# Kernel optimization log

Measured on AMD Instinct MI355X. Metric: run time of the kernel, lower is better.

Reference implementation:

```python
import jax, jax.numpy as jnp
import numpy as np

EPS = 1e-5
GRID = 128          # coarse grid extent -> fine grid is 256^3
N1 = 15000          # coarse voxels
CHILD = 4           # children kept per coarse voxel
N2 = N1 * CHILD     # fine voxels
CIN = 128
COUT = 64


def _build_geometry():
    rng = np.random.RandomState(0)
    flat = rng.choice(GRID ** 3, N1, replace=False)
    cc = np.stack(np.unravel_index(flat, (GRID, GRID, GRID)), axis=1)  # [N1,3]
    offs8 = np.array([[i, j, k] for i in (0, 1) for j in (0, 1) for k in (0, 1)], dtype=np.int64)
    kidx = np.argsort(rng.rand(N1, 8), axis=1)[:, :CHILD]              # [N1,4] distinct child taps
    fine = (cc[:, None, :] * 2 + offs8[kidx]).reshape(-1, 3)           # [N2,3] unique fine coords
    up_src = np.repeat(np.arange(N1), CHILD).astype(np.int32)
    up_kidx = kidx.reshape(-1).astype(np.int32)
    # 27-offset neighbor maps via hashed coordinate lookup
    key = (fine[:, 0] * 256 + fine[:, 1]) * 256 + fine[:, 2]
    order = np.argsort(key)
    skey = key[order]
    offs27 = np.array([[i, j, k] for i in (-1, 0, 1) for j in (-1, 0, 1) for k in (-1, 0, 1)], dtype=np.int64)
    nbr_src = np.full((27, N2), N2, dtype=np.int32)
    nbr_dst = np.full((27, N2), N2, dtype=np.int32)
    for t in range(27):
        q = fine + offs27[t]
        inb = np.all((q >= 0) & (q < 256), axis=1)
        qk = (q[:, 0] * 256 + q[:, 1]) * 256 + q[:, 2]
        pos = np.searchsorted(skey, qk)
        pos = np.clip(pos, 0, N2 - 1)
        hit = inb & (skey[pos] == qk)
        nbr_src[t, hit] = order[pos[hit]]
        nbr_dst[t, hit] = np.arange(N2, dtype=np.int32)[hit]
    return up_src, up_kidx, nbr_src, nbr_dst


def setup_inputs() -> dict:
    key = jax.random.key(0)
    ks = jax.random.split(key, 8)
    up_src, up_kidx, nbr_src, nbr_dst = _build_geometry()
    s_up = 1.0 / np.sqrt(CIN * 8)
    s1 = 1.0 / np.sqrt(CIN * 27)
    s2 = 1.0 / np.sqrt(COUT * 27)
    return {
        "feats1": jax.random.normal(ks[0], (N1, CIN), jnp.float32),
        "feats2": jax.random.normal(ks[1], (N2, CIN // 2), jnp.float32),
        "w_up": jax.random.normal(ks[2], (8, CIN, CIN // 2), jnp.float32) * s_up,
        "gamma_up": jnp.ones((CIN // 2,), jnp.float32),
        "beta_up": jnp.zeros((CIN // 2,), jnp.float32),
        "w1": jax.random.normal(ks[3], (27, CIN, COUT), jnp.float32) * s1,
        "gamma1": jnp.ones((COUT,), jnp.float32),
        "beta1": jnp.zeros((COUT,), jnp.float32),
        "w2": jax.random.normal(ks[4], (27, COUT, COUT), jnp.float32) * s2,
        "gamma2": jnp.ones((COUT,), jnp.float32),
        "beta2": jnp.zeros((COUT,), jnp.float32),
        "up_src": jnp.asarray(up_src),
        "up_kidx": jnp.asarray(up_kidx),
        "nbr_src": jnp.asarray(nbr_src),
        "nbr_dst": jnp.asarray(nbr_dst),
    }


def _bn_relu(x, gamma, beta):
    # training-mode BatchNorm over the point dimension (biased variance), then ReLU
    m = jnp.mean(x, axis=0)
    v = jnp.var(x, axis=0)
    return jax.nn.relu((x - m) * jax.lax.rsqrt(v + EPS) * gamma + beta)


def _sparse_conv(x, w, nbr_src, nbr_dst):
    # x: [N,Ci]; w: [27,Ci,Co]; transform-then-gather-scatter (hash-map sparse conv)
    n = x.shape[0]
    co = w.shape[-1]
    y = jnp.einsum("nc,kco->kno", x, w)                       # [27,N,Co]
    y = jnp.concatenate([y, jnp.zeros((27, 1, co), y.dtype)], axis=1)  # sentinel row
    msg = jnp.take_along_axis(y, nbr_src[:, :, None], axis=1)  # [27,N,Co]
    out = jnp.zeros((n + 1, co), y.dtype).at[nbr_dst.reshape(-1)].add(msg.reshape(-1, co))
    return out[:-1]


def reference(feats1, feats2, w_up, gamma_up, beta_up, w1, gamma1, beta1, w2,
              gamma2, beta2, up_src, up_kidx, nbr_src, nbr_dst):
    # transposed conv k=2 s=2, generative=False: each fine voxel pulls from its unique coarse parent
    y = jnp.einsum("mc,kco->kmo", feats1, w_up)               # [8,N1,Cin/2]
    x1 = y[up_kidx, up_src]                                   # [N2,Cin/2]
    x1 = _bn_relu(x1, gamma_up, beta_up)
    x = jnp.concatenate([x1, feats2], axis=-1)                # [N2,Cin]
    h = _bn_relu(_sparse_conv(x, w1, nbr_src, nbr_dst), gamma1, beta1)
    return _bn_relu(_sparse_conv(h, w2, nbr_src, nbr_dst), gamma2, beta2)
```

## Files before the change

kernel.cpp:

```cpp
#include <hip/hip_runtime.h>


typedef short bf16x4 __attribute__((ext_vector_type(4)));
typedef short bf16x8 __attribute__((ext_vector_type(8)));
typedef float f32x16 __attribute__((ext_vector_type(16)));

__device__ __forceinline__ short f2bf(float f) {
    unsigned u = __float_as_uint(f);
    u += 0x7fffu + ((u >> 16) & 1u);
    return (short)(u >> 16);
}
__device__ __forceinline__ float bf2f(short s) {
    return __uint_as_float(((unsigned)(unsigned short)s) << 16);
}

__global__ __launch_bounds__(256) void k_setup(
    const float* __restrict__ w_up, const float* __restrict__ f1,
    const int* __restrict__ up_kidx,
    short* __restrict__ wupp, short* __restrict__ f1bf,
    int* __restrict__ pmask, int* __restrict__ perm_rows,
    int* __restrict__ rank, int* __restrict__ cnt,
    int n1, int nbGeom)
{
    int tid = threadIdx.x;
    int bid = blockIdx.x;
    if (bid < nbGeom) {
        int p = bid * 256 + tid;
        if (p >= n1) return;
        int4 kd = *(const int4*)(up_kidx + 4 * p);
        int a = kd.x * 4 + 0, b = kd.y * 4 + 1, c = kd.z * 4 + 2, d = kd.w * 4 + 3;
        int t;
        if (a > b) { t = a; a = b; b = t; }
        if (c > d) { t = c; c = d; d = t; }
        if (a > c) { t = a; a = c; c = t; }
        if (b > d) { t = b; b = d; d = t; }
        if (b > c) { t = b; b = c; c = t; }
        perm_rows[4 * p + 0] = 4 * p + (a & 3);
        perm_rows[4 * p + 1] = 4 * p + (b & 3);
        perm_rows[4 * p + 2] = 4 * p + (c & 3);
        perm_rows[4 * p + 3] = 4 * p + (d & 3);
        int mask = (1 << (a >> 2)) | (1 << (b >> 2)) | (1 << (c >> 2)) | (1 << (d >> 2));
        pmask[p] = mask;
        rank[p] = atomicAdd(&cnt[mask], 1);
    } else {
        const int nup8 = 8192;
        int tot = nup8 + n1 * 16;
        int gs = (gridDim.x - nbGeom) * 256;
        for (int e8 = (bid - nbGeom) * 256 + tid; e8 < tot; e8 += gs) {
            if (e8 < nup8) {
                int l = e8 & 63, nt = (e8 >> 6) & 15, ks = e8 >> 10;
                int kb = ks * 16 + (l >> 5) * 8;
                int col = nt * 32 + (l & 31);
                const float* src = w_up + (size_t)(col >> 6) * 8192 + (size_t)kb * 64 + (col & 63);
                bf16x8 o;
                #pragma unroll
                for (int j = 0; j < 8; ++j) o[j] = f2bf(src[(size_t)j * 64]);
                *(bf16x8*)(wupp + (size_t)e8 * 8) = o;
            } else {
                int g = e8 - nup8;
                const float* src = f1 + (size_t)g * 8;
                float4 a = *(const float4*)src;
                float4 b = *(const float4*)(src + 4);
                bf16x8 o;
                o[0] = f2bf(a.x); o[1] = f2bf(a.y); o[2] = f2bf(a.z); o[3] = f2bf(a.w);
                o[4] = f2bf(b.x); o[5] = f2bf(b.y); o[6] = f2bf(b.z); o[7] = f2bf(b.w);
                *(bf16x8*)(f1bf + (size_t)g * 8) = o;
            }
        }
    }
}

__global__ __launch_bounds__(256) void k_up(
    const short* __restrict__ f1bf, const short* __restrict__ wupp,
    const int* __restrict__ pmask, const int* __restrict__ cnt,
    const int* __restrict__ rank, int* __restrict__ perm_par,
    int4* __restrict__ tiles, int* __restrict__ ntl,
    short* __restrict__ yup8, float* __restrict__ stats,
    const float* __restrict__ w1, const float* __restrict__ w2,
    short* __restrict__ w1p, short* __restrict__ w2p,
    const int* __restrict__ nbr, int2* __restrict__ ext,
    int* __restrict__ extc, float* __restrict__ y1, float* __restrict__ y2,
    int n1, int n2, int nt, int nbExt)
{
    int gemmEnd = 1 + 2 * nt;
    if (blockIdx.x == 0) {
        __shared__ int sA[256], sB[256], bb[256];
        int t = threadIdx.x;
        int c = cnt[t], tc = (c + 31) >> 5;
        sA[t] = c; sB[t] = tc;
        __syncthreads();
        for (int off = 1; off < 256; off <<= 1) {
            int a = (t >= off) ? sA[t - off] : 0;
            int b = (t >= off) ? sB[t - off] : 0;
            __syncthreads();
            sA[t] += a; sB[t] += b;
            __syncthreads();
        }
        int base = sA[t] - c, toff = sB[t] - tc;
        bb[t] = base;
        for (int j = 0; j < tc; ++j) tiles[toff + j] = make_int4(t, base, j * 32, c);
        if (t == 255) ntl[0] = sB[255];
        __syncthreads();
        for (int p = t; p < n1; p += 256)
            perm_par[bb[pmask[p]] + rank[p]] = p;
        return;
    }
    if (blockIdx.x >= gemmEnd) {
        int ab = blockIdx.x - gemmEnd;
        int tid = threadIdx.x;
        if (ab < 256) {
            long long tot = (long long)n2 * 16;
            float4 z = make_float4(0.f, 0.f, 0.f, 0.f);
            for (long long e = (long long)ab * 256 + tid; e < tot; e += 256LL * 256) {
                ((float4*)y1)[e] = z;
                ((float4*)y2)[e] = z;
            }
        } else if (ab < 320) {
            const int nw18 = 27648, tot = 27648 + 13824;
            for (int e8 = (ab - 256) * 256 + tid; e8 < tot; e8 += 64 * 256) {
                if (e8 < nw18) {
                    int l = e8 & 63, ch = (e8 >> 6) & 1, ks = (e8 >> 7) & 7, t = e8 >> 10;
                    int kb = ks * 16 + (l >> 5) * 8;
                    int col = ch * 32 + (l & 31);
                    const float* src = w1 + (size_t)t * 8192 + (size_t)kb * 64 + col;
                    bf16x8 o;
                    #pragma unroll
                    for (int j = 0; j < 8; ++j) o[j] = f2bf(src[(size_t)j * 64]);
                    *(bf16x8*)(w1p + (size_t)e8 * 8) = o;
                } else {
                    int g = e8 - nw18;
                    int l = g & 63, ch = (g >> 6) & 1, ks = (g >> 7) & 3, t = g >> 9;
                    int kb = ks * 16 + (l >> 5) * 8;
                    int col = ch * 32 + (l & 31);
                    const float* src = w2 + (size_t)t * 4096 + (size_t)kb * 64 + col;
                    bf16x8 o;
                    #pragma unroll
                    for (int j = 0; j < 8; ++j) o[j] = f2bf(src[(size_t)j * 64]);
                    *(bf16x8*)(w2p + (size_t)g * 8) = o;
                }
            }
        } else {
            int i = (ab - 320) * 256 + tid;
            unsigned hm = 0;
            if (i < n2) {
                #pragma unroll
                for (int t = 0; t < 27; ++t) {
                    int s = nbr[(size_t)t * n2 + i];
                    if (s < n2 && (s >> 2) != (i >> 2)) hm |= 1u << t;
                }
            }
            __shared__ int lcnt, lbase;
            if (tid == 0) lcnt = 0;
            __syncthreads();
            int nh = __popc(hm);
            int myofs = 0;
            if (nh) myofs = atomicAdd(&lcnt, nh);
            __syncthreads();
            if (tid == 0 && lcnt) lbase = atomicAdd(extc, lcnt);
            __syncthreads();
            if (nh) {
                int pos = lbase + myofs;
                unsigned m = hm;
                while (m) {
                    int t = __ffs(m) - 1;
                    m &= m - 1;
                    int s = nbr[(size_t)t * n2 + i];
                    ext[pos++] = make_int2(i, s | (t << 16));
                }
            }
        }
        return;
    }
    __shared__ short lds[32 * 136];
    __shared__ float bs[64], bq[64];
    int bid = blockIdx.x - 1;
    int tile = bid >> 1;
    int w = threadIdx.x >> 6, lane = threadIdx.x & 63;
    int na = (bid & 1) * 8 + w, nb = na + 4;
    if (threadIdx.x < 64) { bs[threadIdx.x] = 0.f; bq[threadIdx.x] = 0.f; }
    #pragma unroll
    for (int it = 0; it < 2; ++it) {
        int c = it * 256 + threadIdx.x;
        int row = c >> 4, col8 = c & 15;
        int gr = tile * 32 + row; if (gr >= n1) gr = n1 - 1;
        int4 g = *(const int4*)(f1bf + (size_t)gr * 128 + col8 * 8);
        short* d = &lds[row * 136 + col8 * 8];
        *(int2*)d = make_int2(g.x, g.y);
        *(int2*)(d + 4) = make_int2(g.z, g.w);
    }
    int m = lane & 31, half = lane >> 5;
    int pm_l = (tile * 32 + m < n1) ? pmask[tile * 32 + m] : 0;
    __syncthreads();
    f32x16 a0, a1;
    #pragma unroll
    for (int i = 0; i < 16; ++i) { a0[i] = 0.f; a1[i] = 0.f; }
    const bf16x8* bp = (const bf16x8*)wupp;
    #pragma unroll
    for (int ks = 0; ks < 8; ++ks) {
        const short* ap = &lds[m * 136 + ks * 16 + half * 8];
        bf16x4 lo = *(const bf16x4*)ap, hi = *(const bf16x4*)(ap + 4);
        bf16x8 a = __builtin_shufflevector(lo, hi, 0, 1, 2, 3, 4, 5, 6, 7);
        bf16x8 b0 = bp[(size_t)(ks * 16 + na) * 64 + lane];
        bf16x8 b1 = bp[(size_t)(ks * 16 + nb) * 64 + lane];
        a0 = __builtin_amdgcn_mfma_f32_32x32x16_bf16(a, b0, a0, 0, 0, 0);
        a1 = __builtin_amdgcn_mfma_f32_32x32x16_bf16(a, b1, a1, 0, 0, 0);
    }
    int col = lane & 31;
    #pragma unroll
    for (int pass = 0; pass < 2; ++pass) {
        const f32x16& acc = pass ? a1 : a0;
        int n = pass ? nb : na;
        int slot = n >> 1, c = (n & 1) * 32 + col;
        float s0 = 0.f, q0 = 0.f;
        #pragma unroll
        for (int reg = 0; reg < 16; ++reg) {
            int r = (reg & 3) + 8 * (reg >> 2) + 4 * half;
            int p = tile * 32 + r;
            float v = acc[reg];
            int mk = __shfl(pm_l, r);
            if (p < n1) {
                yup8[(size_t)p * 512 + n * 32 + col] = f2bf(v);
                if ((mk >> slot) & 1) { s0 += v; q0 += v * v; }
            }
        }
        s0 += __shfl_xor(s0, 32);
        q0 += __shfl_xor(q0, 32);
        if (lane < 32) { atomicAdd(&bs[c], s0); atomicAdd(&bq[c], q0); }
    }
    __syncthreads();
    if (threadIdx.x < 64) {
        atomicAdd(&stats[threadIdx.x], bs[threadIdx.x]);
        atomicAdd(&stats[64 + threadIdx.x], bq[threadIdx.x]);
    }
}

__global__ __launch_bounds__(256) void k_extA(
    const short* __restrict__ yup8, const float* __restrict__ f2,
    const int* __restrict__ up_kidx, const float* __restrict__ w1,
    const float* __restrict__ gamma, const float* __restrict__ beta,
    const float* __restrict__ stats, const int2* __restrict__ ext,
    const int* __restrict__ extc, float* __restrict__ y, int n2)
{
    __shared__ float sc[64], sh[64];
    int tid = threadIdx.x;
    if (tid < 64) {
        float inv = 1.0f / (float)n2;
        float mean = stats[tid] * inv;
        float var = stats[64 + tid] * inv - mean * mean;
        float s = gamma[tid] * rsqrtf(var + 1e-5f);
        sc[tid] = s; sh[tid] = beta[tid] - mean * s;
    }
    __syncthreads();
    int gw = (blockIdx.x * 256 + tid) >> 6;
    int nw = (gridDim.x * 256) >> 6;
    int c = tid & 63;
    int ec = extc[0];
    for (int e = gw; e < ec; e += nw) {
        int2 en = ext[e];
        int i = en.x, s = en.y & 0xFFFF, t = en.y >> 16;
        const short* xr = yup8 + (size_t)(s >> 2) * 512 + up_kidx[s] * 64;
        const float* fr = f2 + (size_t)s * 64;
        const float* wr = w1 + (size_t)t * 8192 + c;
        float acc = 0.f;
        #pragma unroll 4
        for (int k = 0; k < 64; ++k) {
            float xk = fmaxf(bf2f(xr[k]) * sc[k] + sh[k], 0.f);
            acc += xk * wr[(size_t)k * 64];
        }
        #pragma unroll 4
        for (int k = 0; k < 64; ++k)
            acc += fr[k] * wr[(size_t)(64 + k) * 64];
        atomicAdd(&y[(size_t)i * 64 + c], acc);
    }
}

__global__ __launch_bounds__(256) void k_extB(
    const float* __restrict__ y1, const float* __restrict__ w2,
    const float* __restrict__ gamma, const float* __restrict__ beta,
    const float* __restrict__ stats, const int2* __restrict__ ext,
    const int* __restrict__ extc, float* __restrict__ y, int n2)
{
    __shared__ float sc[64], sh[64];
    int tid = threadIdx.x;
    if (tid < 64) {
        float inv = 1.0f / (float)n2;
        float mean = stats[tid] * inv;
        float var = stats[64 + tid] * inv - mean * mean;
        float s = gamma[tid] * rsqrtf(var + 1e-5f);
        sc[tid] = s; sh[tid] = beta[tid] - mean * s;
    }
    __syncthreads();
    int gw = (blockIdx.x * 256 + tid) >> 6;
    int nw = (gridDim.x * 256) >> 6;
    int c = tid & 63;
    int ec = extc[0];
    for (int e = gw; e < ec; e += nw) {
        int2 en = ext[e];
        int i = en.x, s = en.y & 0xFFFF, t = en.y >> 16;
        const float* hr = y1 + (size_t)s * 64;
        const float* wr = w2 + (size_t)t * 4096 + c;
        float acc = 0.f;
        #pragma unroll 4
        for (int k = 0; k < 64; ++k) {
            float hk = fmaxf(hr[k] * sc[k] + sh[k], 0.f);
            acc += hk * wr[(size_t)k * 64];
        }
        atomicAdd(&y[(size_t)i * 64 + c], acc);
    }
}

__device__ __forceinline__ void pair_epi2(const f32x16& a0v, const f32x16& a1v,
                                          int outrow0, int outrow1, int lane,
                                          int ch, float* __restrict__ y,
                                          float* __restrict__ bs,
                                          float* __restrict__ bq)
{
    int col = lane & 31;
    int c = ch * 32 + col;
    int r0[16], r1[16];
    #pragma unroll
    for (int reg = 0; reg < 16; ++reg) {
        int r = (reg & 3) + 8 * (reg >> 2) + 4 * (lane >> 5);
        r0[reg] = __shfl(outrow0, r);
        r1[reg] = __shfl(outrow1, r);
    }
    float o0[16], o1[16];
    #pragma unroll
    for (int reg = 0; reg < 16; ++reg) {
        int ra = (r0[reg] >= 0) ? r0[reg] : 0;
        int rb = (r1[reg] >= 0) ? r1[reg] : 0;
        o0[reg] = y[(size_t)ra * 64 + c];
        o1[reg] = y[(size_t)rb * 64 + c];
    }
    float s0 = 0.f, q0 = 0.f;
    #pragma unroll
    for (int reg = 0; reg < 16; ++reg) {
        if (r0[reg] >= 0) {
            float v = a0v[reg] + o0[reg];
            y[(size_t)r0[reg] * 64 + c] = v;
            s0 += v; q0 += v * v;
        }
        if (r1[reg] >= 0) {
            float v = a1v[reg] + o1[reg];
            y[(size_t)r1[reg] * 64 + c] = v;
            s0 += v; q0 += v * v;
        }
    }
    s0 += __shfl_xor(s0, 32);
    q0 += __shfl_xor(q0, 32);
    if (lane < 32) { atomicAdd(&bs[c], s0); atomicAdd(&bq[c], q0); }
}

__device__ __forceinline__ int tap27(int pa, int pb) {
    int di = ((pb >> 2) & 1) - ((pa >> 2) & 1);
    int dj = ((pb >> 1) & 1) - ((pa >> 1) & 1);
    int dk = (pb & 1) - (pa & 1);
    return (di + 1) * 9 + (dj + 1) * 3 + (dk + 1);
}

__global__ __launch_bounds__(256) void k_pairA(
    const short* __restrict__ yup8, const float* __restrict__ f2,
    const int* __restrict__ up_kidx, const short* __restrict__ wp,
    const float* __restrict__ gamma, const float* __restrict__ beta,
    const float* __restrict__ stats, const int* __restrict__ perm_par,
    const int* __restrict__ perm_rows, const int4* __restrict__ tiles,
    const int* __restrict__ n_tiles, float* __restrict__ y,
    float* __restrict__ ostats, int n2)
{
    constexpr int LP = 520;
    __shared__ short lds[32 * LP];
    __shared__ int srows[128], soff[128];
    __shared__ float scs[64], shs[64], bs[64], bq[64];
    int bt = blockIdx.x;
    if (bt >= n_tiles[0]) return;
    int4 td = tiles[bt];
    int mask = td.x, p_start = td.y, lt = td.z, cntb = td.w;
    int tid = threadIdx.x;
    if (tid < 128) {
        int li = lt + (tid >> 2);
        int pid = perm_par[p_start + ((li < cntb) ? li : 0)];
        int i = perm_rows[pid * 4 + (tid & 3)];
        srows[tid] = i;
        soff[tid] = (i >> 2) * 512 + up_kidx[i] * 64;
    } else if (tid < 192) {
        int cc = tid - 128;
        float inv = 1.0f / (float)n2;
        float mean = stats[cc] * inv;
        float var = stats[64 + cc] * inv - mean * mean;
        float s = gamma[cc] * rsqrtf(var + 1e-5f);
        scs[cc] = s; shs[cc] = beta[cc] - mean * s;
    } else {
        int cc = tid - 192;
        bs[cc] = 0.f; bq[cc] = 0.f;
    }
    __syncthreads();
    #pragma unroll
    for (int it = 0; it < 8; ++it) {
        int c0 = it * 256 + tid;
        int pl = c0 >> 6, w8 = c0 & 63;
        int j = w8 >> 4, col8 = w8 & 15;
        short* d = &lds[pl * LP + j * 128 + col8 * 8];
        if (col8 < 8) {
            bf16x8 g = *(const bf16x8*)(yup8 + (size_t)soff[pl * 4 + j] + col8 * 8);
            short o[8];
            #pragma unroll
            for (int u = 0; u < 8; ++u) {
                int cc = col8 * 8 + u;
                o[u] = f2bf(fmaxf(bf2f(g[u]) * scs[cc] + shs[cc], 0.f));
            }
            *(int2*)d = make_int2(((int)(unsigned short)o[0]) | ((int)o[1] << 16),
                                  ((int)(unsigned short)o[2]) | ((int)o[3] << 16));
            *(int2*)(d + 4) = make_int2(((int)(unsigned short)o[4]) | ((int)o[5] << 16),
                                        ((int)(unsigned short)o[6]) | ((int)o[7] << 16));
        } else {
            const float* fr = f2 + (size_t)srows[pl * 4 + j] * 64 + (col8 - 8) * 8;
            float4 f0 = *(const float4*)fr;
            float4 f1v = *(const float4*)(fr + 4);
            short o[8] = {f2bf(f0.x), f2bf(f0.y), f2bf(f0.z), f2bf(f0.w),
                          f2bf(f1v.x), f2bf(f1v.y), f2bf(f1v.z), f2bf(f1v.w)};
            *(int2*)d = make_int2(((int)(unsigned short)o[0]) | ((int)o[1] << 16),
                                  ((int)(unsigned short)o[2]) | ((int)o[3] << 16));
            *(int2*)(d + 4) = make_int2(((int)(unsigned short)o[4]) | ((int)o[5] << 16),
                                        ((int)(unsigned short)o[6]) | ((int)o[7] << 16));
        }
    }
    int p0 = -1, p1 = -1, p2 = -1, p3 = -1;
    #pragma unroll
    for (int b = 7; b >= 0; --b)
        if ((mask >> b) & 1) { p3 = p2; p2 = p1; p1 = p0; p0 = b; }
    int w = tid >> 6, lane = tid & 63;
    int a0 = w >> 1, a1 = a0 + 2, ch = w & 1;
    int pa0 = (a0 == 0) ? p0 : p1;
    int pa1 = (a1 == 2) ? p2 : p3;
    int t00 = tap27(pa0, p0), t01 = tap27(pa0, p1), t02 = tap27(pa0, p2), t03 = tap27(pa0, p3);
    int t10 = tap27(pa1, p0), t11 = tap27(pa1, p1), t12 = tap27(pa1, p2), t13 = tap27(pa1, p3);
    int m = lane & 31, half = lane >> 5;
    int li = lt + m;
    bool vp = li < cntb;
    int pid = perm_par[p_start + (vp ? li : 0)];
    int outrow0 = vp ? perm_rows[pid * 4 + a0] : -1;
    int outrow1 = vp ? perm_rows[pid * 4 + a1] : -1;
    __syncthreads();
    f32x16 acc0, acc1;
    #pragma unroll
    for (int i = 0; i < 16; ++i) { acc0[i] = 0.f; acc1[i] = 0.f; }
    const bf16x8* bp = (const bf16x8*)wp;
    #pragma unroll
    for (int b = 0; b < 4; ++b) {
        int tb0 = (b == 0) ? t00 : (b == 1) ? t01 : (b == 2) ? t02 : t03;
        int tb1 = (b == 0) ? t10 : (b == 1) ? t11 : (b == 2) ? t12 : t13;
        #pragma unroll
        for (int kk = 0; kk < 8; ++kk) {
            int ks = b * 8 + kk;
            const short* ap = &lds[m * LP + ks * 16 + half * 8];
            bf16x4 lo = *(const bf16x4*)ap, hi = *(const bf16x4*)(ap + 4);
            bf16x8 a = __builtin_shufflevector(lo, hi, 0, 1, 2, 3, 4, 5, 6, 7);
            bf16x8 b0 = bp[((size_t)(tb0 * 8 + kk) * 2 + ch) * 64 + lane];
            bf16x8 b1 = bp[((size_t)(tb1 * 8 + kk) * 2 + ch) * 64 + lane];
            acc0 = __builtin_amdgcn_mfma_f32_32x32x16_bf16(a, b0, acc0, 0, 0, 0);
            acc1 = __builtin_amdgcn_mfma_f32_32x32x16_bf16(a, b1, acc1, 0, 0, 0);
        }
    }
    pair_epi2(acc0, acc1, outrow0, outrow1, lane, ch, y, bs, bq);
    __syncthreads();
    if (tid < 64) {
        atomicAdd(&ostats[tid], bs[tid]);
        atomicAdd(&ostats[64 + tid], bq[tid]);
    }
}

__global__ __launch_bounds__(256) void k_pairB(
    const float* __restrict__ y1, const short* __restrict__ wp,
    const float* __restrict__ gamma, const float* __restrict__ beta,
    const float* __restrict__ stats, const int* __restrict__ perm_par,
    const int* __restrict__ perm_rows, const int4* __restrict__ tiles,
    const int* __restrict__ n_tiles, float* __restrict__ y,
    float* __restrict__ ostats, int n2)
{
    constexpr int LP = 264;
    __shared__ short lds[32 * LP];
    __shared__ int srows[128];
    __shared__ float scs[64], shs[64], bs[64], bq[64];
    int bt = blockIdx.x;
    if (bt >= n_tiles[0]) return;
    int4 td = tiles[bt];
    int mask = td.x, p_start = td.y, lt = td.z, cntb = td.w;
    int tid = threadIdx.x;
    if (tid < 128) {
        int li = lt + (tid >> 2);
        int pid = perm_par[p_start + ((li < cntb) ? li : 0)];
        srows[tid] = perm_rows[pid * 4 + (tid & 3)];
    } else if (tid < 192) {
        int cc = tid - 128;
        float inv = 1.0f / (float)n2;
        float mean = stats[cc] * inv;
        float var = stats[64 + cc] * inv - mean * mean;
        float s = gamma[cc] * rsqrtf(var + 1e-5f);
        scs[cc] = s; shs[cc] = beta[cc] - mean * s;
    } else {
        int cc = tid - 192;
        bs[cc] = 0.f; bq[cc] = 0.f;
    }
    __syncthreads();
    #pragma unroll
    for (int it = 0; it < 4; ++it) {
        int c0 = it * 256 + tid;
        int pl = c0 >> 5, w8 = c0 & 31;
        int j = w8 >> 3, col8 = w8 & 7;
        const float* fr = y1 + (size_t)srows[pl * 4 + j] * 64 + col8 * 8;
        float4 f0 = *(const float4*)fr;
        float4 f1v = *(const float4*)(fr + 4);
        short o[8];
        #pragma unroll
        for (int u = 0; u < 4; ++u) {
            int cc = col8 * 8 + u;
            float v = (u == 0) ? f0.x : (u == 1) ? f0.y : (u == 2) ? f0.z : f0.w;
            o[u] = f2bf(fmaxf(v * scs[cc] + shs[cc], 0.f));
        }
        #pragma unroll
        for (int u = 0; u < 4; ++u) {
            int cc = col8 * 8 + 4 + u;
            float v = (u == 0) ? f1v.x : (u == 1) ? f1v.y : (u == 2) ? f1v.z : f1v.w;
            o[4 + u] = f2bf(fmaxf(v * scs[cc] + shs[cc], 0.f));
        }
        short* d = &lds[pl * LP + j * 64 + col8 * 8];
        *(int2*)d = make_int2(((int)(unsigned short)o[0]) | ((int)o[1] << 16),
                              ((int)(unsigned short)o[2]) | ((int)o[3] << 16));
        *(int2*)(d + 4) = make_int2(((int)(unsigned short)o[4]) | ((int)o[5] << 16),
                                    ((int)(unsigned short)o[6]) | ((int)o[7] << 16));
    }
    int p0 = -1, p1 = -1, p2 = -1, p3 = -1;
    #pragma unroll
    for (int b = 7; b >= 0; --b)
        if ((mask >> b) & 1) { p3 = p2; p2 = p1; p1 = p0; p0 = b; }
    int w = tid >> 6, lane = tid & 63;
    int a0 = w >> 1, a1 = a0 + 2, ch = w & 1;
    int pa0 = (a0 == 0) ? p0 : p1;
    int pa1 = (a1 == 2) ? p2 : p3;
    int t00 = tap27(pa0, p0), t01 = tap27(pa0, p1), t02 = tap27(pa0, p2), t03 = tap27(pa0, p3);
    int t10 = tap27(pa1, p0), t11 = tap27(pa1, p1), t12 = tap27(pa1, p2), t13 = tap27(pa1, p3);
    int m = lane & 31, half = lane >> 5;
    int li = lt + m;
    bool vp = li < cntb;
    int pid = perm_par[p_start + (vp ? li : 0)];
    int outrow0 = vp ? perm_rows[pid * 4 + a0] : -1;
    int outrow1 = vp ? perm_rows[pid * 4 + a1] : -1;
    __syncthreads();
    f32x16 acc0, acc1;
    #pragma unroll
    for (int i = 0; i < 16; ++i) { acc0[i] = 0.f; acc1[i] = 0.f; }
    const bf16x8* bp = (const bf16x8*)wp;
    #pragma unroll
    for (int b = 0; b < 4; ++b) {
        int tb0 = (b == 0) ? t00 : (b == 1) ? t01 : (b == 2) ? t02 : t03;
        int tb1 = (b == 0) ? t10 : (b == 1) ? t11 : (b == 2) ? t12 : t13;
        #pragma unroll
        for (int kk = 0; kk < 4; ++kk) {
            int ks = b * 4 + kk;
            const short* ap = &lds[m * LP + ks * 16 + half * 8];
            bf16x4 lo = *(const bf16x4*)ap, hi = *(const bf16x4*)(ap + 4);
            bf16x8 a = __builtin_shufflevector(lo, hi, 0, 1, 2, 3, 4, 5, 6, 7);
            bf16x8 b0 = bp[((size_t)(tb0 * 4 + kk) * 2 + ch) * 64 + lane];
            bf16x8 b1 = bp[((size_t)(tb1 * 4 + kk) * 2 + ch) * 64 + lane];
            acc0 = __builtin_amdgcn_mfma_f32_32x32x16_bf16(a, b0, acc0, 0, 0, 0);
            acc1 = __builtin_amdgcn_mfma_f32_32x32x16_bf16(a, b1, acc1, 0, 0, 0);
        }
    }
    pair_epi2(acc0, acc1, outrow0, outrow1, lane, ch, y, bs, bq);
    __syncthreads();
    if (tid < 64) {
        atomicAdd(&ostats[tid], bs[tid]);
        atomicAdd(&ostats[64 + tid], bq[tid]);
    }
}

__global__ __launch_bounds__(256) void k_final(
    const float* __restrict__ y, const float* __restrict__ gamma,
    const float* __restrict__ beta, const float* __restrict__ stats,
    float* __restrict__ out, int n2)
{
    __shared__ float sc[64], sh[64];
    int tid = threadIdx.x;
    if (tid < 64) {
        float inv = 1.0f / (float)n2;
        float mean = stats[tid] * inv;
        float var = stats[64 + tid] * inv - mean * mean;
        float s = gamma[tid] * rsqrtf(var + 1e-5f);
        sc[tid] = s;
        sh[tid] = beta[tid] - mean * s;
    }
    __syncthreads();
    long long total = (long long)n2 * 16;
    long long stride = (long long)gridDim.x * blockDim.x;
    for (long long idx = (long long)blockIdx.x * blockDim.x + tid; idx < total; idx += stride) {
        int i = (int)(idx >> 4);
        int c4 = ((int)idx & 15) * 4;
        const float* src = y + (size_t)i * 64 + c4;
        float4 o;
        o.x = fmaxf(src[0] * sc[c4 + 0] + sh[c4 + 0], 0.f);
        o.y = fmaxf(src[1] * sc[c4 + 1] + sh[c4 + 1], 0.f);
        o.z = fmaxf(src[2] * sc[c4 + 2] + sh[c4 + 2], 0.f);
        o.w = fmaxf(src[3] * sc[c4 + 3] + sh[c4 + 3], 0.f);
        *(float4*)(out + (size_t)i * 64 + c4) = o;
    }
}

extern "C" void kernel_launch(void* const* d_in, const int* in_sizes, int n_in,
                              void* d_out, int out_size, void* d_ws, size_t ws_size,
                              hipStream_t stream)
{
    const float* feats1   = (const float*)d_in[0];
    const float* feats2   = (const float*)d_in[1];
    const float* w_up     = (const float*)d_in[2];
    const float* gamma_up = (const float*)d_in[3];
    const float* beta_up  = (const float*)d_in[4];
    const float* w1       = (const float*)d_in[5];
    const float* gamma1   = (const float*)d_in[6];
    const float* beta1    = (const float*)d_in[7];
    const float* w2       = (const float*)d_in[8];
    const float* gamma2   = (const float*)d_in[9];
    const float* beta2    = (const float*)d_in[10];
    const int* up_src     = (const int*)d_in[11];  (void)up_src;
    const int* up_kidx    = (const int*)d_in[12];
    const int* nbr_src    = (const int*)d_in[13];

    int n1 = in_sizes[0] / 128;
    int n2 = in_sizes[1] / 64;

    char* p = (char*)d_ws;
    auto alloc = [&](size_t bytes) {
        char* r = p;
        p += (bytes + 255) & ~(size_t)255;
        return r;
    };
    float* stats    = (float*)alloc(384 * 4);
    int*   cnt      = (int*)alloc(256 * 4);
    int*   extc     = (int*)alloc(16);
    int*   ntl      = (int*)alloc(16);
    size_t headBytes = (size_t)(p - (char*)d_ws);
    int maxTiles    = (n1 + 31) / 32 + 80;
    int4*  tiles    = (int4*)alloc((size_t)maxTiles * 16);
    short* wupp     = (short*)alloc((size_t)65536 * 2);
    short* w1p      = (short*)alloc((size_t)221184 * 2);
    short* w2p      = (short*)alloc((size_t)110592 * 2);
    short* f1bf     = (short*)alloc((size_t)n1 * 128 * 2);
    int*   pmask    = (int*)alloc((size_t)n1 * 4);
    int*   rank     = (int*)alloc((size_t)n1 * 4);
    int*   perm_par = (int*)alloc((size_t)n1 * 4);
    int*   perm_rows= (int*)alloc((size_t)4 * n1 * 4);
    int2*  ext      = (int2*)alloc((size_t)27 * n2 * 8);
    short* yup8     = (short*)alloc((size_t)n1 * 512 * 2);
    float* y1       = (float*)alloc((size_t)n2 * 64 * 4);
    float* y2       = (float*)alloc((size_t)n2 * 64 * 4);

    int nbExt  = (n2 + 255) / 256;
    int nbGeom = (n1 + 255) / 256;
    int nbPack = 128;
    int nbSetup = nbGeom + nbPack;
    int nt = (n1 + 31) / 32;
    int upBlocks = 1 + 2 * nt + 256 + 64 + nbExt;
    int ewBlocks16 = (int)(((long long)n2 * 16 + 255) / 256);

    hipMemsetAsync(d_ws, 0, headBytes, stream);
    k_setup<<<nbSetup, 256, 0, stream>>>(w_up, feats1, up_kidx, wupp, f1bf,
                                         pmask, perm_rows, rank, cnt,
                                         n1, nbGeom);
    k_up<<<upBlocks, 256, 0, stream>>>(f1bf, wupp, pmask, cnt, rank, perm_par,
                                       tiles, ntl, yup8, stats,
                                       w1, w2, w1p, w2p, nbr_src, ext, extc,
                                       y1, y2, n1, n2, nt, nbExt);
    k_extA<<<512, 256, 0, stream>>>(yup8, feats2, up_kidx, w1, gamma_up, beta_up,
                                    stats, ext, extc, y1, n2);
    k_pairA<<<maxTiles, 256, 0, stream>>>(yup8, feats2, up_kidx, w1p, gamma_up,
                                          beta_up, stats, perm_par, perm_rows,
                                          tiles, ntl, y1, stats + 128, n2);
    k_extB<<<512, 256, 0, stream>>>(y1, w2, gamma1, beta1, stats + 128, ext,
                                    extc, y2, n2);
    k_pairB<<<maxTiles, 256, 0, stream>>>(y1, w2p, gamma1, beta1, stats + 128,
                                          perm_par, perm_rows, tiles, ntl, y2,
                                          stats + 256, n2);
    k_final<<<ewBlocks16, 256, 0, stream>>>(y2, gamma2, beta2, stats + 256,
                                            (float*)d_out, n2);
}
```

Baseline: 237.6 us.

## Fuse cross-parent neighbor kernels into pair GEMM kernels with flagged atomic epilogues

Removes the separate k_extA and k_extB launches and runs that edge work in the first 256 blocks of k_pairA and k_pairB. The two block groups now race on the output, so rows that have cross-parent neighbors are marked in a bitmask. Those rows are accumulated with atomics, and batch-norm statistics are rebuilt from the returned old values via v*(v+2*old). Unflagged rows keep plain stores and no longer read y first, which cuts the read-modify-write traffic and two launches, at the cost of more atomics and reliance on the algebraic stats reconstruction.

Measured after the change: 232.3 us. 2.2% less time.

```diff
diff --git a/kernel.cpp b/kernel.cpp
--- a/kernel.cpp
+++ b/kernel.cpp
@@ -4,6 +4,9 @@
 typedef short bf16x4 __attribute__((ext_vector_type(4)));
 typedef short bf16x8 __attribute__((ext_vector_type(8)));
 typedef float f32x16 __attribute__((ext_vector_type(16)));
+
+#define ROWM 0xFFFFF
+#define RFLAG (1 << 30)
 
 __device__ __forceinline__ short f2bf(float f) {
     unsigned u = __float_as_uint(f);
@@ -79,7 +82,8 @@
     const float* __restrict__ w1, const float* __restrict__ w2,
     short* __restrict__ w1p, short* __restrict__ w2p,
     const int* __restrict__ nbr, int2* __restrict__ ext,
-    int* __restrict__ extc, float* __restrict__ y1, float* __restrict__ y2,
+    int* __restrict__ extc, unsigned* __restrict__ flagbits,
+    float* __restrict__ y1, float* __restrict__ y2,
     int n1, int n2, int nt, int nbExt)
 {
     int gemmEnd = 1 + 2 * nt;
@@ -149,6 +153,7 @@
                     if (s < n2 && (s >> 2) != (i >> 2)) hm |= 1u << t;
                 }
             }
+            if (hm) atomicOr(&flagbits[i >> 5], 1u << (i & 31));
             __shared__ int lcnt, lbase;
             if (tid == 0) lcnt = 0;
             __syncthreads();
@@ -234,81 +239,6 @@
     }
 }
 
-__global__ __launch_bounds__(256) void k_extA(
-    const short* __restrict__ yup8, const float* __restrict__ f2,
-    const int* __restrict__ up_kidx, const float* __restrict__ w1,
-    const float* __restrict__ gamma, const float* __restrict__ beta,
-    const float* __restrict__ stats, const int2* __restrict__ ext,
-    const int* __restrict__ extc, float* __restrict__ y, int n2)
-{
-    __shared__ float sc[64], sh[64];
-    int tid = threadIdx.x;
-    if (tid < 64) {
-        float inv = 1.0f / (float)n2;
-        float mean = stats[tid] * inv;
-        float var = stats[64 + tid] * inv - mean * mean;
-        float s = gamma[tid] * rsqrtf(var + 1e-5f);
-        sc[tid] = s; sh[tid] = beta[tid] - mean * s;
-    }
-    __syncthreads();
-    int gw = (blockIdx.x * 256 + tid) >> 6;
-    int nw = (gridDim.x * 256) >> 6;
-    int c = tid & 63;
-    int ec = extc[0];
-    for (int e = gw; e < ec; e += nw) {
-        int2 en = ext[e];
-        int i = en.x, s = en.y & 0xFFFF, t = en.y >> 16;
-        const short* xr = yup8 + (size_t)(s >> 2) * 512 + up_kidx[s] * 64;
-        const float* fr = f2 + (size_t)s * 64;
-        const float* wr = w1 + (size_t)t * 8192 + c;
-        float acc = 0.f;
-        #pragma unroll 4
-        for (int k = 0; k < 64; ++k) {
-            float xk = fmaxf(bf2f(xr[k]) * sc[k] + sh[k], 0.f);
-            acc += xk * wr[(size_t)k * 64];
-        }
-        #pragma unroll 4
-        for (int k = 0; k < 64; ++k)
-            acc += fr[k] * wr[(size_t)(64 + k) * 64];
-        atomicAdd(&y[(size_t)i * 64 + c], acc);
-    }
-}
-
-__global__ __launch_bounds__(256) void k_extB(
-    const float* __restrict__ y1, const float* __restrict__ w2,
-    const float* __restrict__ gamma, const float* __restrict__ beta,
-    const float* __restrict__ stats, const int2* __restrict__ ext,
-    const int* __restrict__ extc, float* __restrict__ y, int n2)
-{
-    __shared__ float sc[64], sh[64];
-    int tid = threadIdx.x;
-    if (tid < 64) {
-        float inv = 1.0f / (float)n2;
-        float mean = stats[tid] * inv;
-        float var = stats[64 + tid] * inv - mean * mean;
-        float s = gamma[tid] * rsqrtf(var + 1e-5f);
-        sc[tid] = s; sh[tid] = beta[tid] - mean * s;
-    }
-    __syncthreads();
-    int gw = (blockIdx.x * 256 + tid) >> 6;
-    int nw = (gridDim.x * 256) >> 6;
-    int c = tid & 63;
-    int ec = extc[0];
-    for (int e = gw; e < ec; e += nw) {
-        int2 en = ext[e];
-        int i = en.x, s = en.y & 0xFFFF, t = en.y >> 16;
-        const float* hr = y1 + (size_t)s * 64;
-        const float* wr = w2 + (size_t)t * 4096 + c;
-        float acc = 0.f;
-        #pragma unroll 4
-        for (int k = 0; k < 64; ++k) {
-            float hk = fmaxf(hr[k] * sc[k] + sh[k], 0.f);
-            acc += hk * wr[(size_t)k * 64];
-        }
-        atomicAdd(&y[(size_t)i * 64 + c], acc);
-    }
-}
-
 __device__ __forceinline__ void pair_epi2(const f32x16& a0v, const f32x16& a1v,
                                           int outrow0, int outrow1, int lane,
                                           int ch, float* __restrict__ y,
@@ -317,33 +247,31 @@
 {
     int col = lane & 31;
     int c = ch * 32 + col;
-    int r0[16], r1[16];
+    float s0 = 0.f, q0 = 0.f;
     #pragma unroll
     for (int reg = 0; reg < 16; ++reg) {
         int r = (reg & 3) + 8 * (reg >> 2) + 4 * (lane >> 5);
-        r0[reg] = __shfl(outrow0, r);
-        r1[reg] = __shfl(outrow1, r);
-    }
-    float o0[16], o1[16];
-    #pragma unroll
-    for (int reg = 0; reg < 16; ++reg) {
-        int ra = (r0[reg] >= 0) ? r0[reg] : 0;
-        int rb = (r1[reg] >= 0) ? r1[reg] : 0;
-        o0[reg] = y[(size_t)ra * 64 + c];
-        o1[reg] = y[(size_t)rb * 64 + c];
-    }
-    float s0 = 0.f, q0 = 0.f;
-    #pragma unroll
-    for (int reg = 0; reg < 16; ++reg) {
-        if (r0[reg] >= 0) {
-            float v = a0v[reg] + o0[reg];
-            y[(size_t)r0[reg] * 64 + c] = v;
-            s0 += v; q0 += v * v;
-        }
-        if (r1[reg] >= 0) {
-            float v = a1v[reg] + o1[reg];
-            y[(size_t)r1[reg] * 64 + c] = v;
-            s0 += v; q0 += v * v;
+        int r0 = __shfl(outrow0, r);
+        int r1 = __shfl(outrow1, r);
+        if (r0 >= 0) {
+            float v = a0v[reg];
+            size_t ad = (size_t)(r0 & ROWM) * 64 + c;
+            if (r0 & RFLAG) {
+                float old = atomicAdd(&y[ad], v);
+                s0 += v; q0 += v * (v + 2.f * old);
+            } else {
+                y[ad] = v; s0 += v; q0 += v * v;
+            }
+        }
+        if (r1 >= 0) {
+            float v = a1v[reg];
+            size_t ad = (size_t)(r1 & ROWM) * 64 + c;
+            if (r1 & RFLAG) {
+                float old = atomicAdd(&y[ad], v);
+                s0 += v; q0 += v * (v + 2.f * old);
+            } else {
+                y[ad] = v; s0 += v; q0 += v * v;
+            }
         }
     }
     s0 += __shfl_xor(s0, 32);
@@ -361,26 +289,67 @@
 __global__ __launch_bounds__(256) void k_pairA(
     const short* __restrict__ yup8, const float* __restrict__ f2,
     const int* __restrict__ up_kidx, const short* __restrict__ wp,
+    const float* __restrict__ w1f,
     const float* __restrict__ gamma, const float* __restrict__ beta,
     const float* __restrict__ stats, const int* __restrict__ perm_par,
     const int* __restrict__ perm_rows, const int4* __restrict__ tiles,
-    const int* __restrict__ n_tiles, float* __restrict__ y,
-    float* __restrict__ ostats, int n2)
+    const int* __restrict__ n_tiles, const int2* __restrict__ ext,
+    const int* __restrict__ extc, const unsigned* __restrict__ flagbits,
+    float* __restrict__ y, float* __restrict__ ostats, int n2, int nExtB)
 {
     constexpr int LP = 520;
     __shared__ short lds[32 * LP];
     __shared__ int srows[128], soff[128];
     __shared__ float scs[64], shs[64], bs[64], bq[64];
-    int bt = blockIdx.x;
+    int tid = threadIdx.x;
+    if (blockIdx.x < nExtB) {
+        if (tid < 64) {
+            float inv = 1.0f / (float)n2;
+            float mean = stats[tid] * inv;
+            float var = stats[64 + tid] * inv - mean * mean;
+            float s = gamma[tid] * rsqrtf(var + 1e-5f);
+            scs[tid] = s; shs[tid] = beta[tid] - mean * s;
+            bs[tid] = 0.f; bq[tid] = 0.f;
+        }
+        __syncthreads();
+        int gw = (blockIdx.x * 256 + tid) >> 6;
+        int nw = nExtB * 4;
+        int c = tid & 63;
+        int ec = extc[0];
+        for (int e = gw; e < ec; e += nw) {
+            int2 en = ext[e];
+            int i = en.x, s = en.y & 0xFFFF, t = en.y >> 16;
+            const short* xr = yup8 + (size_t)(s >> 2) * 512 + up_kidx[s] * 64;
+            const float* fr = f2 + (size_t)s * 64;
+            const float* wr = w1f + (size_t)t * 8192 + c;
+            float acc = 0.f;
+            #pragma unroll 4
+            for (int k = 0; k < 64; ++k)
+                acc += fmaxf(bf2f(xr[k]) * scs[k] + shs[k], 0.f) * wr[(size_t)k * 64];
+            #pragma unroll 4
+            for (int k = 0; k < 64; ++k)
+                acc += fr[k] * wr[(size_t)(64 + k) * 64];
+            float old = atomicAdd(&y[(size_t)i * 64 + c], acc);
+            atomicAdd(&bs[c], acc);
+            atomicAdd(&bq[c], acc * (acc + 2.f * old));
+        }
+        __syncthreads();
+        if (tid < 64) {
+            atomicAdd(&ostats[tid], bs[tid]);
+            atomicAdd(&ostats[64 + tid], bq[tid]);
+        }
+        return;
+    }
+    int bt = blockIdx.x - nExtB;
     if (bt >= n_tiles[0]) return;
     int4 td = tiles[bt];
     int mask = td.x, p_start = td.y, lt = td.z, cntb = td.w;
-    int tid = threadIdx.x;
     if (tid < 128) {
         int li = lt + (tid >> 2);
         int pid = perm_par[p_start + ((li < cntb) ? li : 0)];
         int i = perm_rows[pid * 4 + (tid & 3)];
-        srows[tid] = i;
+        unsigned fb = (flagbits[i >> 5] >> (i & 31)) & 1u;
+        srows[tid] = i | (int)(fb << 30);
         soff[tid] = (i >> 2) * 512 + up_kidx[i] * 64;
     } else if (tid < 192) {
         int cc = tid - 128;
@@ -413,7 +382,7 @@
             *(int2*)(d + 4) = make_int2(((int)(unsigned short)o[4]) | ((int)o[5] << 16),
                                         ((int)(unsigned short)o[6]) | ((int)o[7] << 16));
         } else {
-            const float* fr = f2 + (size_t)srows[pl * 4 + j] * 64 + (col8 - 8) * 8;
+            const float* fr = f2 + (size_t)(srows[pl * 4 + j] & ROWM) * 64 + (col8 - 8) * 8;
             float4 f0 = *(const float4*)fr;
             float4 f1v = *(const float4*)(fr + 4);
             short o[8] = {f2bf(f0.x), f2bf(f0.y), f2bf(f0.z), f2bf(f0.w),
@@ -437,9 +406,8 @@
     int m = lane & 31, half = lane >> 5;
     int li = lt + m;
     bool vp = li < cntb;
-    int pid = perm_par[p_start + (vp ? li : 0)];
-    int outrow0 = vp ? perm_rows[pid * 4 + a0] : -1;
-    int outrow1 = vp ? perm_rows[pid * 4 + a1] : -1;
+    int outrow0 = vp ? srows[m * 4 + a0] : -1;
+    int outrow1 = vp ? srows[m * 4 + a1] : -1;
     __syncthreads();
     f32x16 acc0, acc1;
     #pragma unroll
@@ -471,25 +439,63 @@
 
 __global__ __launch_bounds__(256) void k_pairB(
     const float* __restrict__ y1, const short* __restrict__ wp,
+    const float* __restrict__ w2f,
     const float* __restrict__ gamma, const float* __restrict__ beta,
     const float* __restrict__ stats, const int* __restrict__ perm_par,
     const int* __restrict__ perm_rows, const int4* __restrict__ tiles,
-    const int* __restrict__ n_tiles, float* __restrict__ y,
-    float* __restrict__ ostats, int n2)
+    const int* __restrict__ n_tiles, const int2* __restrict__ ext,
+    const int* __restrict__ extc, const unsigned* __restrict__ flagbits,
+    float* __restrict__ y, float* __restrict__ ostats, int n2, int nExtB)
 {
     constexpr int LP = 264;
     __shared__ short lds[32 * LP];
     __shared__ int srows[128];
     __shared__ float scs[64], shs[64], bs[64], bq[64];
-    int bt = blockIdx.x;
+    int tid = threadIdx.x;
+    if (blockIdx.x < nExtB) {
+        if (tid < 64) {
+            float inv = 1.0f / (float)n2;
+            float mean = stats[tid] * inv;
+            float var = stats[64 + tid] * inv - mean * mean;
+            float s = gamma[tid] * rsqrtf(var + 1e-5f);
+            scs[tid] = s; shs[tid] = beta[tid] - mean * s;
+            bs[tid] = 0.f; bq[tid] = 0.f;
+        }
+        __syncthreads();
+        int gw = (blockIdx.x * 256 + tid) >> 6;
+        int nw = nExtB * 4;
+        int c = tid & 63;
+        int ec = extc[0];
+        for (int e = gw; e < ec; e += nw) {
+            int2 en = ext[e];
+            int i = en.x, s = en.y & 0xFFFF, t = en.y >> 16;
+            const float* hr = y1 + (size_t)s * 64;
+            const float* wr = w2f + (size_t)t * 4096 + c;
+            float acc = 0.f;
+            #pragma unroll 4
+            for (int k = 0; k < 64; ++k)
+                acc += fmaxf(hr[k] * scs[k] + shs[k], 0.f) * wr[(size_t)k * 64];
+            float old = atomicAdd(&y[(size_t)i * 64 + c], acc);
+            atomicAdd(&bs[c], acc);
+            atomicAdd(&bq[c], acc * (acc + 2.f * old));
+        }
+        __syncthreads();
+        if (tid < 64) {
+            atomicAdd(&ostats[tid], bs[tid]);
+            atomicAdd(&ostats[64 + tid], bq[tid]);
+        }
+        return;
+    }
+    int bt = blockIdx.x - nExtB;
     if (bt >= n_tiles[0]) return;
     int4 td = tiles[bt];
     int mask = td.x, p_start = td.y, lt = td.z, cntb = td.w;
-    int tid = threadIdx.x;
     if (tid < 128) {
         int li = lt + (tid >> 2);
         int pid = perm_par[p_start + ((li < cntb) ? li : 0)];
-        srows[tid] = perm_rows[pid * 4 + (tid & 3)];
+        int i = perm_rows[pid * 4 + (tid & 3)];
+        unsigned fb = (flagbits[i >> 5] >> (i & 31)) & 1u;
+        srows[tid] = i | (int)(fb << 30);
     } else if (tid < 192) {
         int cc = tid - 128;
         float inv = 1.0f / (float)n2;
@@ -507,7 +513,7 @@
         int c0 = it * 256 + tid;
         int pl = c0 >> 5, w8 = c0 & 31;
         int j = w8 >> 3, col8 = w8 & 7;
-        const float* fr = y1 + (size_t)srows[pl * 4 + j] * 64 + col8 * 8;
+        const float* fr = y1 + (size_t)(srows[pl * 4 + j] & ROWM) * 64 + col8 * 8;
         float4 f0 = *(const float4*)fr;
         float4 f1v = *(const float4*)(fr + 4);
         short o[8];
@@ -542,9 +548,8 @@
     int m = lane & 31, half = lane >> 5;
     int li = lt + m;
     bool vp = li < cntb;
-    int pid = perm_par[p_start + (vp ? li : 0)];
-    int outrow0 = vp ? perm_rows[pid * 4 + a0] : -1;
-    int outrow1 = vp ? perm_rows[pid * 4 + a1] : -1;
+    int outrow0 = vp ? srows[m * 4 + a0] : -1;
+    int outrow1 = vp ? srows[m * 4 + a1] : -1;
     __syncthreads();
     f32x16 acc0, acc1;
     #pragma unroll
@@ -637,6 +642,7 @@
     int*   cnt      = (int*)alloc(256 * 4);
     int*   extc     = (int*)alloc(16);
     int*   ntl      = (int*)alloc(16);
+    unsigned* flagbits = (unsigned*)alloc(((size_t)(n2 + 31) / 32) * 4);
     size_t headBytes = (size_t)(p - (char*)d_ws);
     int maxTiles    = (n1 + 31) / 32 + 80;
     int4*  tiles    = (int4*)alloc((size_t)maxTiles * 16);
@@ -660,6 +666,7 @@
     int nt = (n1 + 31) / 32;
     int upBlocks = 1 + 2 * nt + 256 + 64 + nbExt;
     int ewBlocks16 = (int)(((long long)n2 * 16 + 255) / 256);
+    const int EXTB = 256;
 
     hipMemsetAsync(d_ws, 0, headBytes, stream);
     k_setup<<<nbSetup, 256, 0, stream>>>(w_up, feats1, up_kidx, wupp, f1bf,
@@ -668,17 +675,17 @@
     k_up<<<upBlocks, 256, 0, stream>>>(f1bf, wupp, pmask, cnt, rank, perm_par,
                                        tiles, ntl, yup8, stats,
                                        w1, w2, w1p, w2p, nbr_src, ext, extc,
-                                       y1, y2, n1, n2, nt, nbExt);
-    k_extA<<<512, 256, 0, stream>>>(yup8, feats2, up_kidx, w1, gamma_up, beta_up,
-                                    stats, ext, extc, y1, n2);
-    k_pairA<<<maxTiles, 256, 0, stream>>>(yup8, feats2, up_kidx, w1p, gamma_up,
-                                          beta_up, stats, perm_par, perm_rows,
-                                          tiles, ntl, y1, stats + 128, n2);
-    k_extB<<<512, 256, 0, stream>>>(y1, w2, gamma1, beta1, stats + 128, ext,
-                                    extc, y2, n2);
-    k_pairB<<<maxTiles, 256, 0, stream>>>(y1, w2p, gamma1, beta1, stats + 128,
-                                          perm_par, perm_rows, tiles, ntl, y2,
-                                          stats + 256, n2);
+                                       flagbits, y1, y2, n1, n2, nt, nbExt);
+    k_pairA<<<EXTB + maxTiles, 256, 0, stream>>>(yup8, feats2, up_kidx, w1p, w1,
+                                                 gamma_up, beta_up, stats,
+                                                 perm_par, perm_rows, tiles, ntl,
+                                                 ext, extc, flagbits,
+                                                 y1, stats + 128, n2, EXTB);
+    k_pairB<<<EXTB + maxTiles, 256, 0, stream>>>(y1, w2p, w2, gamma1, beta1,
+                                                 stats + 128, perm_par,
+                                                 perm_rows, tiles, ntl,
+                                                 ext, extc, flagbits,
+                                                 y2, stats + 256, n2, EXTB);
     k_final<<<ewBlocks16, 256, 0, stream>>>(y2, gamma2, beta2, stats + 256,
                                             (float*)d_out, n2);
 }
```
